# Kernel tuning notes

Hardware: AMD Instinct MI355X
Metric: run time of the kernel (lower is better)

Reference implementation:

```python
import jax, jax.numpy as jnp
import numpy as np
import math

B, L, S, E, D = 32, 2048, 2048, 64, 64

def setup_inputs() -> dict:
    key = jax.random.key(0)
    kq, kk, kv = jax.random.split(key, 3)
    return {
        "queries": jax.random.normal(kq, (B, L, E), dtype=jnp.float32),
        "keys":    jax.random.normal(kk, (B, S, E), dtype=jnp.float32),
        "values":  jax.random.normal(kv, (B, S, D), dtype=jnp.float32),
    }

def reference(queries, keys, values):
    # scale = 1/sqrt(E) since self.scale is None
    scale = 1.0 / math.sqrt(queries.shape[-1])
    # unfused QK^T -> softmax -> V (dropout is identity at inference)
    scores = jnp.einsum('ble,bse->bls', queries, keys)  # [B,L,S]
    # mask_flag branch not taken because L == S (matches torch code path)
    A = jax.nn.softmax(scale * scores, axis=-1)
    V = jnp.einsum('bls,bsd->bld', A, values)  # [B,L,D]
    return V
```

## Files before the change

kernel.cpp:

```cpp
#include <hip/hip_runtime.h>
#include <hip/hip_bf16.h>


#define B_ 32
#define L_ 2048
#define S_ 2048
#define E_ 64
#define D_ 64
#define BQ 128
#define NIMG 32
#define IMG_BYTES 16384
#define NCHUNK 16

typedef __attribute__((ext_vector_type(8))) short bf16x8;
typedef __attribute__((ext_vector_type(16))) float f32x16;
typedef __attribute__((ext_vector_type(4))) unsigned u32x4;

__device__ __forceinline__ unsigned short f2b(float f) {
  unsigned u = __builtin_bit_cast(unsigned, f);
  u += 0x7fff + ((u >> 16) & 1);
  return (unsigned short)(u >> 16);
}

__device__ __forceinline__ unsigned pk2(float a, float b) {
#if defined(__has_builtin) && __has_builtin(__builtin_amdgcn_cvt_pk_bf16_f32)
  typedef __bf16 b2 __attribute__((ext_vector_type(2)));
  b2 t = __builtin_amdgcn_cvt_pk_bf16_f32(a, b);
  return __builtin_bit_cast(unsigned, t);
#else
  return (unsigned)f2b(a) | ((unsigned)f2b(b) << 16);
#endif
}

__device__ __forceinline__ float fexp2(float x) {
#if defined(__has_builtin) && __has_builtin(__builtin_amdgcn_exp2f)
  return __builtin_amdgcn_exp2f(x);
#else
  return exp2f(x);
#endif
}

__device__ __forceinline__ void cp16(const void* g, void* lbase) {
#if defined(__has_builtin) && __has_builtin(__builtin_amdgcn_global_load_lds)
  typedef const __attribute__((address_space(1))) void gvoid;
  typedef __attribute__((address_space(3))) void lvoid;
  __builtin_amdgcn_global_load_lds((gvoid*)g, (lvoid*)lbase, 16, 0, 0);
#endif
}

__global__ __launch_bounds__(256) void prepass(
    const float* __restrict__ K, const float* __restrict__ V,
    char* __restrict__ ws) {
  __shared__ __align__(16) short vimg[4096];

  const int tid  = threadIdx.x;
  const int lane = tid & 63;
  const int quad = lane >> 4;
  const int qb0  = quad & 1;
  const int qb1  = (quad >> 1) & 1;

  const int b  = blockIdx.x >> 5;
  const int c  = blockIdx.x & 31;
  const int s0 = c * 64;

  const float* Kb = K + (long)b * S_ * E_;
  const float* Vb = V + (long)b * S_ * D_;
  short* img = (short*)(ws + (size_t)blockIdx.x * IMG_BYTES);

#pragma unroll
  for (int it = 0; it < 4; ++it) {
    const int i  = tid + it * 256;
    const int s  = i >> 4;
    const int c4 = (i & 15) << 2;

    float4 kv = *(const float4*)(Kb + (long)(s0 + s) * E_ + c4);
    {
      int g = (c4 >> 3) ^ (s & 7);
      *(uint2*)&img[s * 64 + g * 8 + (c4 & 7)] = make_uint2(pk2(kv.x, kv.y), pk2(kv.z, kv.w));
    }

    float4 vv = *(const float4*)(Vb + (long)(s0 + s) * D_ + c4);
    float a0 = vv.x, a1 = vv.y, a2 = vv.z, a3 = vv.w;
    float s0f = qb1 ? a0 : a2;
    float s1f = qb1 ? a1 : a3;
    float r0  = __shfl_xor(s0f, 32);
    float r1  = __shfl_xor(s1f, 32);
    float b0 = qb1 ? r0 : a0;
    float b1 = qb1 ? r1 : a1;
    float b2 = qb1 ? a2 : r0;
    float b3 = qb1 ? a3 : r1;
    float t0 = qb0 ? b0 : b1;
    float t1 = qb0 ? b2 : b3;
    float u0 = __shfl_xor(t0, 16);
    float u1 = __shfl_xor(t1, 16);
    float w0 = qb0 ? u0 : b0;
    float w1 = qb0 ? b1 : u0;
    float w2 = qb0 ? u1 : b2;
    float w3 = qb0 ? b3 : u1;
    const int base = s - quad;
    const int d    = c4 + quad;
    int g = (base >> 3) ^ (d & 7);
    *(uint2*)&vimg[d * 64 + g * 8 + (base & 7)] = make_uint2(pk2(w0, w1), pk2(w2, w3));
  }

  __syncthreads();

  {
    const int tau = tid >> 5;
    const int u2  = (tid & 31) << 1;
    const int mt  = tau >> 2;
    const int s16 = tau & 3;
#pragma unroll
    for (int lam = 0; lam < 2; ++lam) {
      const int l    = u2 + lam;
      const int hh   = l >> 5;
      const int l31v = l & 31;
      const int d    = mt * 32 + l31v;
      const int oct  = s16 * 2 + hh;
      const int g    = oct ^ (d & 7);
      const float4 frag = *(const float4*)&vimg[d * 64 + g * 8];
      *(float4*)((char*)img + 8192 + tau * 1024 + l * 16) = frag;
    }
  }
}

__global__ __launch_bounds__(512, 4) void attn_fwd(
    const float* __restrict__ Q, const char* __restrict__ ws,
    float* __restrict__ O) {
  __shared__ __align__(16) char smem[35840];
  float* Obuf = (float*)smem;
  float* ML   = (float*)(smem + 34816);

  const int tid  = threadIdx.x;
  const int lane = tid & 63;
  const int wv   = tid >> 6;
  const int l31  = lane & 31;
  const int h    = lane >> 5;
  const int qg   = wv >> 1;
  const int kh   = wv & 1;

  const int i_ = blockIdx.x;
  const int x_ = i_ & 7;
  const int j_ = i_ >> 3;
  const int b  = (x_ << 2) | (j_ >> 4);
  const int q0 = (j_ & 15) * BQ;

  const float SCALE2 = 0.125f * 1.44269504088896340736f;
  const char* img0 = ws + (size_t)b * ((size_t)NIMG * IMG_BYTES);

#pragma unroll
  for (int j = 0; j < 2; ++j)
    cp16(img0 + (wv >> 2) * 16384 + (wv & 3) * 2048 + j * 1024 + lane * 16,
         smem + wv * 2048 + j * 1024);

  const char* vgb = img0 + kh * 16384 + 8192 + 4096 + lane * 16;

  bf16x8 qf[4];
  {
    const float* qrow = Q + ((long)b * L_ + q0 + qg * 32 + l31) * E_;
#pragma unroll
    for (int ke = 0; ke < 4; ++ke) {
      const float* sp = qrow + ke * 16 + h * 8;
      float4 x = *(const float4*)(sp);
      float4 y = *(const float4*)(sp + 4);
      u32x4 uu = { pk2(x.x * SCALE2, x.y * SCALE2), pk2(x.z * SCALE2, x.w * SCALE2),
                   pk2(y.x * SCALE2, y.y * SCALE2), pk2(y.z * SCALE2, y.w * SCALE2) };
      qf[ke] = __builtin_bit_cast(bf16x8, uu);
    }
  }

  int pl = l31;
  {
    const int blk = (pl >> 2) & 3;
    if (blk == 1) pl += 4;
    else if (blk == 2) pl -= 4;
  }

  const int kb = kh * 8192 + (pl << 7) + ((h ^ (pl & 7)) << 4);

  f32x16 o[2];
#pragma unroll
  for (int mt = 0; mt < 2; ++mt)
#pragma unroll
    for (int r = 0; r < 16; ++r) o[mt][r] = 0.f;
  float lrun = 0.f;

  __syncthreads();

#define CHUNK_BODY(TT, BUFB, OTHB)                                             \
  {                                                                            \
    if ((TT) + 1 < NCHUNK) {                                                   \
      const char* img = img0 + (size_t)(2 * ((TT) + 1) + (wv >> 2)) * 16384;   \
      _Pragma("unroll")                                                        \
      for (int j = 0; j < 2; ++j)                                              \
        cp16(img + (wv & 3) * 2048 + j * 1024 + lane * 16,                     \
             smem + (OTHB) + wv * 2048 + j * 1024);                            \
    }                                                                          \
    const char* vp = vgb + (size_t)(TT) * 32768;                               \
    _Pragma("unroll")                                                          \
    for (int nt = 0; nt < 2; ++nt) {                                           \
          \
      bf16x8 v00 = *(const bf16x8*)(vp + (((nt * 2 + 0) << 10) - 4096));       \
      bf16x8 v01 = *(const bf16x8*)(vp + (((nt * 2 + 1) << 10) - 4096));       \
      bf16x8 v10 = *(const bf16x8*)(vp + (((4 + nt * 2 + 0) << 10) - 4096));   \
      bf16x8 v11 = *(const bf16x8*)(vp + (((4 + nt * 2 + 1) << 10) - 4096));   \
      bf16x8 kf[4];                                                            \
      _Pragma("unroll")                                                        \
      for (int ke = 0; ke < 4; ++ke)                                           \
        kf[ke] = *(const bf16x8*)(smem +                                       \
                   (kb ^ ((BUFB) | (nt << 12) | (ke << 5))));                  \
      f32x16 acc;                                                              \
      _Pragma("unroll")                                                        \
      for (int r = 0; r < 16; ++r) acc[r] = 0.f;                               \
      __builtin_amdgcn_s_setprio(1);                                           \
      _Pragma("unroll")                                                        \
      for (int ke = 0; ke < 4; ++ke)                                           \
        acc = __builtin_amdgcn_mfma_f32_32x32x16_bf16(kf[ke], qf[ke], acc,     \
                                                      0, 0, 0);                \
      __builtin_amdgcn_s_setprio(0);                                           \
      u32x4 f0, f1;                                                            \
      _Pragma("unroll")                                                        \
      for (int gixx = 0; gixx < 4; ++gixx) {                                   \
        float p0 = fexp2(acc[2 * gixx]);                                       \
        float p1 = fexp2(acc[2 * gixx + 1]);                                   \
        float p2 = fexp2(acc[8 + 2 * gixx]);                                   \
        float p3 = fexp2(acc[8 + 2 * gixx + 1]);                               \
        f0[gixx] = pk2(p0, p1);                                                \
        f1[gixx] = pk2(p2, p3);                                                \
        lrun += (p0 + p1) + (p2 + p3);                                         \
      }                                                                        \
      bf16x8 pf0 = __builtin_bit_cast(bf16x8, f0);                             \
      bf16x8 pf1 = __builtin_bit_cast(bf16x8, f1);                             \
      __builtin_amdgcn_s_setprio(1);                                           \
      o[0] = __builtin_amdgcn_mfma_f32_32x32x16_bf16(v00, pf0, o[0], 0, 0, 0); \
      o[1] = __builtin_amdgcn_mfma_f32_32x32x16_bf16(v10, pf0, o[1], 0, 0, 0); \
      o[0] = __builtin_amdgcn_mfma_f32_32x32x16_bf16(v01, pf1, o[0], 0, 0, 0); \
      o[1] = __builtin_amdgcn_mfma_f32_32x32x16_bf16(v11, pf1, o[1], 0, 0, 0); \
      __builtin_amdgcn_s_setprio(0);                                           \
    }                                                                          \
    __syncthreads();                                                           \
  }

  for (int t = 0; t < NCHUNK; t += 2) {
    CHUNK_BODY(t, 0, 16384)
    CHUNK_BODY(t + 1, 16384, 0)
  }
#undef CHUNK_BODY

  float lt = lrun + __shfl_xor(lrun, 32);

  if (lane < 32)
    ML[(qg * 2 + kh) * 32 + l31] = lt;
  __syncthreads();

  const float inv = 1.f / (lt + ML[(qg * 2 + (kh ^ 1)) * 32 + l31]);
  const int q = qg * 32 + l31;

  if (kh == 1) {
#pragma unroll
    for (int mt = 0; mt < 2; ++mt)
#pragma unroll
      for (int r = 0; r < 16; ++r) {
        const int d = mt * 32 + (r & 3) + 8 * (r >> 2) + 4 * h;
        Obuf[q * 68 + d] = o[mt][r];
      }
  }
  __syncthreads();

  if (kh == 0) {
#pragma unroll
    for (int mt = 0; mt < 2; ++mt)
#pragma unroll
      for (int r = 0; r < 16; ++r) {
        const int d = mt * 32 + (r & 3) + 8 * (r >> 2) + 4 * h;
        Obuf[q * 68 + d] = (o[mt][r] + Obuf[q * 68 + d]) * inv;
      }
  }
  __syncthreads();

  {
    const int qq = tid >> 2;
    const int dh = (tid & 3) * 16;
    float* orow = O + ((long)b * L_ + q0 + qq) * D_ + dh;
    const float* src = &Obuf[qq * 68 + dh];
#pragma unroll
    for (int j = 0; j < 4; ++j)
      *(float4*)(orow + j * 4) = *(const float4*)(src + j * 4);
  }
}

extern "C" void kernel_launch(void* const* d_in, const int* in_sizes, int n_in,
                              void* d_out, int out_size, void* d_ws, size_t ws_size,
                              hipStream_t stream) {
  const float* Q = (const float*)d_in[0];
  const float* K = (const float*)d_in[1];
  const float* V = (const float*)d_in[2];
  float* O = (float*)d_out;

  prepass<<<dim3(B_ * NIMG), dim3(256), 0, stream>>>(K, V, (char*)d_ws);
  attn_fwd<<<dim3(B_ * (L_ / BQ)), dim3(512), 0, stream>>>(Q, (const char*)d_ws, O);
}
```

Baseline: 147.8 us.

## Pre-lay K in MFMA fragment order and load K directly from global

The prepass now writes K in per-lane MFMA fragment order, the same way V already was. The main kernel drops the async global-to-LDS double-buffered K staging and its per-chunk barriers, and loads K fragments straight from global/L2 with coalesced 16-byte loads. This removes LDS traffic and block-wide synchronisation from the inner loop. In exchange it loses the explicit prefetch overlap and relies on cache and hardware latency hiding for the global loads.

```diff
diff --git a/kernel.cpp b/kernel.cpp
--- a/kernel.cpp
+++ b/kernel.cpp
@@ -40,17 +40,10 @@
 #endif
 }
 
-__device__ __forceinline__ void cp16(const void* g, void* lbase) {
-#if defined(__has_builtin) && __has_builtin(__builtin_amdgcn_global_load_lds)
-  typedef const __attribute__((address_space(1))) void gvoid;
-  typedef __attribute__((address_space(3))) void lvoid;
-  __builtin_amdgcn_global_load_lds((gvoid*)g, (lvoid*)lbase, 16, 0, 0);
-#endif
-}
-
 __global__ __launch_bounds__(256) void prepass(
     const float* __restrict__ K, const float* __restrict__ V,
     char* __restrict__ ws) {
+  __shared__ __align__(16) short kimg[4096];
   __shared__ __align__(16) short vimg[4096];
 
   const int tid  = threadIdx.x;
@@ -75,8 +68,16 @@
 
     float4 kv = *(const float4*)(Kb + (long)(s0 + s) * E_ + c4);
     {
-      int g = (c4 >> 3) ^ (s & 7);
-      *(uint2*)&img[s * 64 + g * 8 + (c4 & 7)] = make_uint2(pk2(kv.x, kv.y), pk2(kv.z, kv.w));
+      const int r31 = s & 31;
+      int p31 = r31;
+      const int blk = (p31 >> 2) & 3;
+      if (blk == 1) p31 += 4;
+      else if (blk == 2) p31 -= 4;
+      const int nt = s >> 5;
+      const int ke = c4 >> 4;
+      const int hh = (c4 >> 3) & 1;
+      const int idx = (nt * 4 + ke) * 512 + (hh * 32 + p31) * 8 + (c4 & 7);
+      *(uint2*)&kimg[idx] = make_uint2(pk2(kv.x, kv.y), pk2(kv.z, kv.w));
     }
 
     float4 vv = *(const float4*)(Vb + (long)(s0 + s) * D_ + c4);
@@ -106,6 +107,13 @@
   __syncthreads();
 
   {
+    const char* src = (const char*)kimg + tid * 32;
+    char* dst = (char*)img + tid * 32;
+    *(float4*)(dst)      = *(const float4*)(src);
+    *(float4*)(dst + 16) = *(const float4*)(src + 16);
+  }
+
+  {
     const int tau = tid >> 5;
     const int u2  = (tid & 31) << 1;
     const int mt  = tau >> 2;
@@ -148,12 +156,8 @@
   const float SCALE2 = 0.125f * 1.44269504088896340736f;
   const char* img0 = ws + (size_t)b * ((size_t)NIMG * IMG_BYTES);
 
-#pragma unroll
-  for (int j = 0; j < 2; ++j)
-    cp16(img0 + (wv >> 2) * 16384 + (wv & 3) * 2048 + j * 1024 + lane * 16,
-         smem + wv * 2048 + j * 1024);
-
-  const char* vgb = img0 + kh * 16384 + 8192 + 4096 + lane * 16;
+  const char* kp = img0 + kh * 16384 + lane * 16 + 4096;
+  const char* vp = kp + 8192;
 
   bf16x8 qf[4];
   {
@@ -169,15 +173,6 @@
     }
   }
 
-  int pl = l31;
-  {
-    const int blk = (pl >> 2) & 3;
-    if (blk == 1) pl += 4;
-    else if (blk == 2) pl -= 4;
-  }
-
-  const int kb = kh * 8192 + (pl << 7) + ((h ^ (pl & 7)) << 4);
-
   f32x16 o[2];
 #pragma unroll
   for (int mt = 0; mt < 2; ++mt)
@@ -185,67 +180,49 @@
     for (int r = 0; r < 16; ++r) o[mt][r] = 0.f;
   float lrun = 0.f;
 
-  __syncthreads();
-
-#define CHUNK_BODY(TT, BUFB, OTHB)                                             \
-  {                                                                            \
-    if ((TT) + 1 < NCHUNK) {                                                   \
-      const char* img = img0 + (size_t)(2 * ((TT) + 1) + (wv >> 2)) * 16384;   \
-      _Pragma("unroll")                                                        \
-      for (int j = 0; j < 2; ++j)                                              \
-        cp16(img + (wv & 3) * 2048 + j * 1024 + lane * 16,                     \
-             smem + (OTHB) + wv * 2048 + j * 1024);                            \
-    }                                                                          \
-    const char* vp = vgb + (size_t)(TT) * 32768;                               \
-    _Pragma("unroll")                                                          \
-    for (int nt = 0; nt < 2; ++nt) {                                           \
-          \
-      bf16x8 v00 = *(const bf16x8*)(vp + (((nt * 2 + 0) << 10) - 4096));       \
-      bf16x8 v01 = *(const bf16x8*)(vp + (((nt * 2 + 1) << 10) - 4096));       \
-      bf16x8 v10 = *(const bf16x8*)(vp + (((4 + nt * 2 + 0) << 10) - 4096));   \
-      bf16x8 v11 = *(const bf16x8*)(vp + (((4 + nt * 2 + 1) << 10) - 4096));   \
-      bf16x8 kf[4];                                                            \
-      _Pragma("unroll")                                                        \
-      for (int ke = 0; ke < 4; ++ke)                                           \
-        kf[ke] = *(const bf16x8*)(smem +                                       \
-                   (kb ^ ((BUFB) | (nt << 12) | (ke << 5))));                  \
-      f32x16 acc;                                                              \
-      _Pragma("unroll")                                                        \
-      for (int r = 0; r < 16; ++r) acc[r] = 0.f;                               \
-      __builtin_amdgcn_s_setprio(1);                                           \
-      _Pragma("unroll")                                                        \
-      for (int ke = 0; ke < 4; ++ke)                                           \
-        acc = __builtin_amdgcn_mfma_f32_32x32x16_bf16(kf[ke], qf[ke], acc,     \
-                                                      0, 0, 0);                \
-      __builtin_amdgcn_s_setprio(0);                                           \
-      u32x4 f0, f1;                                                            \
-      _Pragma("unroll")                                                        \
-      for (int gixx = 0; gixx < 4; ++gixx) {                                   \
-        float p0 = fexp2(acc[2 * gixx]);                                       \
-        float p1 = fexp2(acc[2 * gixx + 1]);                                   \
-        float p2 = fexp2(acc[8 + 2 * gixx]);                                   \
-        float p3 = fexp2(acc[8 + 2 * gixx + 1]);                               \
-        f0[gixx] = pk2(p0, p1);                                                \
-        f1[gixx] = pk2(p2, p3);                                                \
-        lrun += (p0 + p1) + (p2 + p3);                                         \
-      }                                                                        \
-      bf16x8 pf0 = __builtin_bit_cast(bf16x8, f0);                             \
-      bf16x8 pf1 = __builtin_bit_cast(bf16x8, f1);                             \
-      __builtin_amdgcn_s_setprio(1);                                           \
-      o[0] = __builtin_amdgcn_mfma_f32_32x32x16_bf16(v00, pf0, o[0], 0, 0, 0); \
-      o[1] = __builtin_amdgcn_mfma_f32_32x32x16_bf16(v10, pf0, o[1], 0, 0, 0); \
-      o[0] = __builtin_amdgcn_mfma_f32_32x32x16_bf16(v01, pf1, o[0], 0, 0, 0); \
-      o[1] = __builtin_amdgcn_mfma_f32_32x32x16_bf16(v11, pf1, o[1], 0, 0, 0); \
-      __builtin_amdgcn_s_setprio(0);                                           \
-    }                                                                          \
-    __syncthreads();                                                           \
-  }
-
-  for (int t = 0; t < NCHUNK; t += 2) {
-    CHUNK_BODY(t, 0, 16384)
-    CHUNK_BODY(t + 1, 16384, 0)
-  }
-#undef CHUNK_BODY
+  for (int t = 0; t < NCHUNK; ++t) {
+#pragma unroll
+    for (int nt = 0; nt < 2; ++nt) {
+      bf16x8 kf0 = *(const bf16x8*)(kp + ((nt * 4 + 0) * 1024 - 4096));
+      bf16x8 kf1 = *(const bf16x8*)(kp + ((nt * 4 + 1) * 1024 - 4096));
+      bf16x8 kf2 = *(const bf16x8*)(kp + ((nt * 4 + 2) * 1024 - 4096));
+      bf16x8 kf3 = *(const bf16x8*)(kp + ((nt * 4 + 3) * 1024 - 4096));
+      f32x16 acc;
+#pragma unroll
+      for (int r = 0; r < 16; ++r) acc[r] = 0.f;
+      __builtin_amdgcn_s_setprio(1);
+      acc = __builtin_amdgcn_mfma_f32_32x32x16_bf16(kf0, qf[0], acc, 0, 0, 0);
+      acc = __builtin_amdgcn_mfma_f32_32x32x16_bf16(kf1, qf[1], acc, 0, 0, 0);
+      acc = __builtin_amdgcn_mfma_f32_32x32x16_bf16(kf2, qf[2], acc, 0, 0, 0);
+      acc = __builtin_amdgcn_mfma_f32_32x32x16_bf16(kf3, qf[3], acc, 0, 0, 0);
+      __builtin_amdgcn_s_setprio(0);
+      bf16x8 v00 = *(const bf16x8*)(vp + ((0 + nt * 2 + 0) * 1024 - 4096));
+      bf16x8 v01 = *(const bf16x8*)(vp + ((0 + nt * 2 + 1) * 1024 - 4096));
+      bf16x8 v10 = *(const bf16x8*)(vp + ((4 + nt * 2 + 0) * 1024 - 4096));
+      bf16x8 v11 = *(const bf16x8*)(vp + ((4 + nt * 2 + 1) * 1024 - 4096));
+      u32x4 f0, f1;
+#pragma unroll
+      for (int gix = 0; gix < 4; ++gix) {
+        float p0 = fexp2(acc[2 * gix]);
+        float p1 = fexp2(acc[2 * gix + 1]);
+        float p2 = fexp2(acc[8 + 2 * gix]);
+        float p3 = fexp2(acc[8 + 2 * gix + 1]);
+        f0[gix] = pk2(p0, p1);
+        f1[gix] = pk2(p2, p3);
+        lrun += (p0 + p1) + (p2 + p3);
+      }
+      bf16x8 pf0 = __builtin_bit_cast(bf16x8, f0);
+      bf16x8 pf1 = __builtin_bit_cast(bf16x8, f1);
+      __builtin_amdgcn_s_setprio(1);
+      o[0] = __builtin_amdgcn_mfma_f32_32x32x16_bf16(v00, pf0, o[0], 0, 0, 0);
+      o[1] = __builtin_amdgcn_mfma_f32_32x32x16_bf16(v10, pf0, o[1], 0, 0, 0);
+      o[0] = __builtin_amdgcn_mfma_f32_32x32x16_bf16(v01, pf1, o[0], 0, 0, 0);
+      o[1] = __builtin_amdgcn_mfma_f32_32x32x16_bf16(v11, pf1, o[1], 0, 0, 0);
+      __builtin_amdgcn_s_setprio(0);
+    }
+    kp += 32768;
+    vp += 32768;
+  }
 
   float lt = lrun + __shfl_xor(lrun, 32);
 
```

Result: faster. 143.7 us (-2.8%).
